# Kernel tuning notes

Hardware: AMD Instinct MI355X
Metric: run time of the kernel (lower is better)

## Reference

```python
import jax, jax.numpy as jnp
import numpy as np

EMBED = 1024
HEADS = 16
HEAD_DIM = EMBED // HEADS


def setup_inputs() -> dict:
    key = jax.random.key(0)
    k1, k2, k3, k4, k5 = jax.random.split(key, 5)
    B, S, E = 4, 2048, EMBED
    scale = 1.0 / np.sqrt(E)
    return {
        "tensor": jax.random.normal(k1, (B, S, E), dtype=jnp.float32),
        "in_proj_w": jax.random.normal(k2, (3 * E, E), dtype=jnp.float32) * scale,
        "in_proj_b": jax.random.normal(k3, (3 * E,), dtype=jnp.float32) * 0.02,
        "out_proj_w": jax.random.normal(k4, (E, E), dtype=jnp.float32) * scale,
        "out_proj_b": jax.random.normal(k5, (E,), dtype=jnp.float32) * 0.02,
        "causal_mask": 1,
    }


def reference(tensor, in_proj_w, in_proj_b, out_proj_w, out_proj_b, causal_mask):
    B, S, E = tensor.shape
    H, D = HEADS, HEAD_DIM
    # fused qkv projection (torch Linear: x @ W.T + b)
    qkv = tensor @ in_proj_w.T + in_proj_b  # [B, S, 3E]
    q, k, v = jnp.split(qkv, 3, axis=-1)
    # [B, S, E] -> [B, H, S, D]
    q = q.reshape(B, S, H, D).transpose(0, 2, 1, 3)
    k = k.reshape(B, S, H, D).transpose(0, 2, 1, 3)
    v = v.reshape(B, S, H, D).transpose(0, 2, 1, 3)
    scores = jnp.einsum("bhqd,bhkd->bhqk", q, k)  # [B, H, S, S]
    if causal_mask:
        mask = jnp.triu(jnp.ones((S, S), dtype=bool), k=1)
        scores = jnp.where(mask, -jnp.inf, scores)
    scores = scores / np.sqrt(D).astype(np.float32)
    attn = jax.nn.softmax(scores, axis=-1)
    out = jnp.einsum("bhqk,bhkd->bhqd", attn, v)  # [B, H, S, D]
    out = out.transpose(0, 2, 1, 3).reshape(B, S, E)
    return out @ out_proj_w.T + out_proj_b
```

## Files before the change

### kernel.cpp

```cpp
#include <hip/hip_runtime.h>
#include <hip/hip_bf16.h>

#define B_  4
#define S_  2048
#define E_  1024
#define H_  16
#define D_  64
#define M_  (B_*S_)
#define N3_ (3*E_)

typedef __bf16 bf16;
typedef bf16  bf16x4 __attribute__((ext_vector_type(4)));
typedef bf16  bf16x8 __attribute__((ext_vector_type(8)));
typedef float f32x4  __attribute__((ext_vector_type(4)));

#define SC2 0.18033688011112043f

__device__ __forceinline__ f32x4 mfma16(bf16x8 a, bf16x8 b, f32x4 c) {
    return __builtin_amdgcn_mfma_f32_16x16x32_bf16(a, b, c, 0, 0, 0);
}

typedef const __attribute__((address_space(1))) void* gas_t;
typedef __attribute__((address_space(3))) void* las_t;
__device__ __forceinline__ void gl_lds16(const void* g, void* l) {
    __builtin_amdgcn_global_load_lds((gas_t)g, (las_t)l, 16, 0, 0);
}

#define WAITCNT_VM4() __builtin_amdgcn_s_waitcnt(0x0F74)
#define WAITCNT_VM2() __builtin_amdgcn_s_waitcnt(0x0F72)
#define WAITCNT_VM0() __builtin_amdgcn_s_waitcnt(0x0F70)

__global__ __launch_bounds__(256) void cvt_all(const float* __restrict__ x,
                                               const float* __restrict__ w_in,
                                               const float* __restrict__ w_out,
                                               bf16* __restrict__ Xbf,
                                               bf16* __restrict__ Wqkv,
                                               bf16* __restrict__ Wo) {
    const int n1 = M_ * E_ / 4, n2 = N3_ * E_ / 4, n3 = E_ * E_ / 4;
    int i = blockIdx.x * blockDim.x + threadIdx.x;
    const float* src; bf16* dst; int j;
    if (i < n1)           { src = x;     dst = Xbf;  j = i; }
    else if (i < n1 + n2) { src = w_in;  dst = Wqkv; j = i - n1; }
    else if (i < n1 + n2 + n3) { src = w_out; dst = Wo; j = i - n1 - n2; }
    else return;
    float4 v = *(const float4*)(src + (size_t)j * 4);
    bf16x4 o;
    o[0] = (bf16)v.x; o[1] = (bf16)v.y; o[2] = (bf16)v.z; o[3] = (bf16)v.w;
    *(bf16x4*)(dst + (size_t)j * 4) = o;
}

__global__ __launch_bounds__(256) void gemm_qkv(const bf16* __restrict__ X,
                                                const bf16* __restrict__ W,
                                                const float* __restrict__ bias,
                                                bf16* __restrict__ QKV,
                                                bf16* __restrict__ Vt) {
    __shared__ __align__(16) bf16 As[128 * 64];
    __shared__ __align__(16) bf16 Bs[128 * 64];
    const int t = threadIdx.x;
    const int wav = t >> 6, lane = t & 63, quad = lane >> 4, l15 = lane & 15;
    const int m0 = blockIdx.y * 128, n0 = blockIdx.x * 128;
    const int wr = (wav >> 1) * 64, wc = (wav & 1) * 64;
    const int srow = t >> 3;
    const int swz  = ((t & 7) ^ (srow & 7)) * 8;
    const bool isV = (n0 >= 2 * E_);

    const bf16* Ablk = X + (size_t)m0 * E_;
    const bf16* Bblk = W + (size_t)n0 * E_;
    f32x4 acc[4][4] = {};

    for (int kk = 0; kk < E_; kk += 64) {
        __syncthreads();
        #pragma unroll
        for (int ps = 0; ps < 4; ++ps) {
            gl_lds16(Ablk + (size_t)(srow + ps * 32) * E_ + kk + swz, As + (size_t)(t + ps * 256) * 8);
            gl_lds16(Bblk + (size_t)(srow + ps * 32) * E_ + kk + swz, Bs + (size_t)(t + ps * 256) * 8);
        }
        __syncthreads();
        #pragma unroll
        for (int ks = 0; ks < 2; ++ks) {
            bf16x8 af[4], bw[4];
            #pragma unroll
            for (int i = 0; i < 4; ++i) {
                const int ra = wr + i * 16 + l15;
                const int rb = wc + i * 16 + l15;
                const int cx = ((ks * 4 + quad) ^ (l15 & 7)) * 8;
                af[i] = *(const bf16x8*)&As[ra * 64 + cx];
                bw[i] = *(const bf16x8*)&Bs[rb * 64 + cx];
            }
            if (!isV) {
                #pragma unroll
                for (int i = 0; i < 4; ++i)
                    #pragma unroll
                    for (int j = 0; j < 4; ++j)
                        acc[i][j] = mfma16(af[i], bw[j], acc[i][j]);
            } else {
                #pragma unroll
                for (int i = 0; i < 4; ++i)
                    #pragma unroll
                    for (int j = 0; j < 4; ++j)
                        acc[i][j] = mfma16(bw[i], af[j], acc[i][j]);
            }
        }
    }
    if (!isV) {
        #pragma unroll
        for (int i = 0; i < 4; ++i)
            #pragma unroll
            for (int j = 0; j < 4; ++j)
                #pragma unroll
                for (int r = 0; r < 4; ++r) {
                    int mg = m0 + wr + i * 16 + quad * 4 + r;
                    int ng = n0 + wc + j * 16 + l15;
                    float v = acc[i][j][r] + bias[ng];
                    int which = ng >> 10, rem = ng & 1023;
                    if (which == 0) v *= SC2;
                    int h = rem >> 6, d = rem & 63;
                    int b = mg >> 11, s = mg & 2047;
                    QKV[(size_t)which * (B_ * H_ * S_ * D_) +
                        (((size_t)(b * H_ + h) * S_ + s) * D_ + d)] = (bf16)v;
                }
    } else {
        #pragma unroll
        for (int i = 0; i < 4; ++i)
            #pragma unroll
            for (int j = 0; j < 4; ++j)
                #pragma unroll
                for (int r = 0; r < 4; ++r) {
                    int ng = n0 + wc + i * 16 + quad * 4 + r;
                    int mg = m0 + wr + j * 16 + l15;
                    float v = acc[i][j][r] + bias[ng];
                    int rem = ng & 1023;
                    int h = rem >> 6, d = rem & 63;
                    int b = mg >> 11, s = mg & 2047;
                    Vt[(((size_t)(b * H_ + h) * D_ + d) * S_) + s] = (bf16)v;
                }
    }
}

__global__ __launch_bounds__(512, 4) void attn8(const bf16* __restrict__ Q,
                                                const bf16* __restrict__ K,
                                                const bf16* __restrict__ Vt,
                                                bf16* __restrict__ O) {
    __shared__ __align__(16) bf16 Ks[2][64 * 64];
    __shared__ __align__(16) bf16 Vs[2][64 * 64];
    __shared__ __align__(16) bf16 Ps[8][16 * 64];

    const int t = threadIdx.x;
    const int wav = t >> 6, lane = t & 63, quad = lane >> 4, l15 = lane & 15;
    const int p  = blockIdx.x >> 6;
    const int bh = blockIdx.x & 63;

    const bf16* Qb = Q  + (size_t)bh * S_ * D_;
    const bf16* Kb = K  + (size_t)bh * S_ * D_;
    const bf16* Vb = Vt + (size_t)bh * (size_t)D_ * S_;

    const int srow = t >> 3;
    const int swz  = ((t & 7) ^ (srow & 7)) * 8;
    bf16* Pw = &Ps[wav][0];
    const int pswz = l15 & 7;

    const int b = bh >> 4, h = bh & 15;

    #pragma unroll 1
    for (int phase = 0; phase < 2; ++phase) {
        const int qb  = phase ? (15 - p) : p;
        const int q0w = qb * 128 + wav * 16;
        const int qg  = q0w + l15;
        const int niter = 2 * qb + 2;

        __builtin_amdgcn_s_barrier();
        gl_lds16(Kb + (size_t)srow * D_ + swz, &Ks[0][(size_t)t * 8]);
        gl_lds16(Vb + (size_t)srow * S_ + swz, &Vs[0][(size_t)t * 8]);

        bf16x8 qf0 = *(const bf16x8*)&Qb[(size_t)(q0w + l15) * D_ + quad * 8];
        bf16x8 qf1 = *(const bf16x8*)&Qb[(size_t)(q0w + l15) * D_ + 32 + quad * 8];

        f32x4 oacc[4] = {};
        f32x4 psum = {0.f, 0.f, 0.f, 0.f};

        #pragma unroll 1
        for (int it = 0; it < niter; ++it) {
            const int key0 = it * 64;
            const int cur = it & 1;
            const bf16* Kc = &Ks[cur][0];
            const bf16* Vc = &Vs[cur][0];

            __builtin_amdgcn_s_barrier();
            if (it + 1 < niter) {
                const int kn = key0 + 64;
                gl_lds16(Kb + (size_t)(kn + srow) * D_ + swz, &Ks[1 - cur][(size_t)t * 8]);
                gl_lds16(Vb + (size_t)srow * S_ + kn + swz,   &Vs[1 - cur][(size_t)t * 8]);
                WAITCNT_VM2();
            } else {
                WAITCNT_VM0();
            }
            __builtin_amdgcn_s_barrier();

            f32x4 sacc[4];
            #pragma unroll
            for (int mt = 0; mt < 4; ++mt) {
                const int krow = mt * 16 + l15;
                const int sw = krow & 7;
                bf16x8 kf0 = *(const bf16x8*)&Kc[krow * 64 + ((quad ^ sw) * 8)];
                bf16x8 kf1 = *(const bf16x8*)&Kc[krow * 64 + (((4 + quad) ^ sw) * 8)];
                f32x4 a = {};
                a = mfma16(kf0, qf0, a);
                a = mfma16(kf1, qf1, a);
                sacc[mt] = a;
            }

            #pragma unroll
            for (int mt = 0; mt < 4; ++mt) {
                if (key0 + mt * 16 + 15 > q0w) {
                    #pragma unroll
                    for (int r = 0; r < 4; ++r) {
                        int key = key0 + mt * 16 + quad * 4 + r;
                        sacc[mt][r] = (key > qg) ? -3e38f : sacc[mt][r];
                    }
                }
            }

            #pragma unroll
            for (int mt = 0; mt < 4; ++mt) {
                bf16x4 pk;
                #pragma unroll
                for (int r = 0; r < 4; ++r) {
                    float pv = __builtin_amdgcn_exp2f(sacc[mt][r]);
                    psum[r] += pv;
                    pk[r] = (bf16)pv;
                }
                const int pc = ((mt * 2 + (quad >> 1)) ^ pswz) * 8 + (quad & 1) * 4;
                *(bf16x4*)&Pw[l15 * 64 + pc] = pk;
            }

            bf16x8 pf0 = *(const bf16x8*)&Pw[l15 * 64 + ((quad ^ pswz) * 8)];
            bf16x8 pf1 = *(const bf16x8*)&Pw[l15 * 64 + (((4 + quad) ^ pswz) * 8)];
            #pragma unroll
            for (int nt = 0; nt < 4; ++nt) {
                const int vrow = nt * 16 + l15;
                const int sw = vrow & 7;
                bf16x8 vf0 = *(const bf16x8*)&Vc[vrow * 64 + ((quad ^ sw) * 8)];
                bf16x8 vf1 = *(const bf16x8*)&Vc[vrow * 64 + (((4 + quad) ^ sw) * 8)];
                oacc[nt] = mfma16(pf0, vf0, oacc[nt]);
                oacc[nt] = mfma16(pf1, vf1, oacc[nt]);
            }
        }

        float rsum = psum[0] + psum[1] + psum[2] + psum[3];
        rsum += __shfl_xor(rsum, 16);
        rsum += __shfl_xor(rsum, 32);
        const float linv = 1.0f / rsum;

        #pragma unroll
        for (int rr = 0; rr < 4; ++rr) {
            float li = __shfl(linv, quad * 4 + rr);
            const int q = q0w + quad * 4 + rr;
            #pragma unroll
            for (int nt = 0; nt < 4; ++nt)
                O[((size_t)b * S_ + q) * E_ + h * D_ + nt * 16 + l15] =
                    (bf16)(oacc[nt][rr] * li);
        }
    }
}

__global__ __launch_bounds__(256) void gemm_out(const bf16* __restrict__ A,
                                                const bf16* __restrict__ W,
                                                const float* __restrict__ bias,
                                                float* __restrict__ out) {
    __shared__ __align__(16) bf16 As[128 * 64];
    __shared__ __align__(16) bf16 Bs[128 * 64];
    const int t = threadIdx.x;
    const int wav = t >> 6, lane = t & 63, quad = lane >> 4, l15 = lane & 15;
    const int m0 = blockIdx.y * 128, n0 = blockIdx.x * 128;
    const int wr = (wav >> 1) * 64, wc = (wav & 1) * 64;
    const int srow = t >> 3;
    const int swz  = ((t & 7) ^ (srow & 7)) * 8;

    const bf16* Ablk = A + (size_t)m0 * E_;
    const bf16* Bblk = W + (size_t)n0 * E_;
    f32x4 acc[4][4] = {};

    for (int kk = 0; kk < E_; kk += 64) {
        __syncthreads();
        #pragma unroll
        for (int ps = 0; ps < 4; ++ps) {
            gl_lds16(Ablk + (size_t)(srow + ps * 32) * E_ + kk + swz, As + (size_t)(t + ps * 256) * 8);
            gl_lds16(Bblk + (size_t)(srow + ps * 32) * E_ + kk + swz, Bs + (size_t)(t + ps * 256) * 8);
        }
        __syncthreads();
        #pragma unroll
        for (int ks = 0; ks < 2; ++ks) {
            bf16x8 af[4], bw[4];
            #pragma unroll
            for (int i = 0; i < 4; ++i) {
                const int ra = wr + i * 16 + l15;
                const int rb = wc + i * 16 + l15;
                const int cx = ((ks * 4 + quad) ^ (l15 & 7)) * 8;
                af[i] = *(const bf16x8*)&As[ra * 64 + cx];
                bw[i] = *(const bf16x8*)&Bs[rb * 64 + cx];
            }
            #pragma unroll
            for (int i = 0; i < 4; ++i)
                #pragma unroll
                for (int j = 0; j < 4; ++j)
                    acc[i][j] = mfma16(af[i], bw[j], acc[i][j]);
        }
    }
    #pragma unroll
    for (int i = 0; i < 4; ++i)
        #pragma unroll
        for (int j = 0; j < 4; ++j)
            #pragma unroll
            for (int r = 0; r < 4; ++r) {
                int mg = m0 + wr + i * 16 + quad * 4 + r;
                int ng = n0 + wc + j * 16 + l15;
                out[(size_t)mg * E_ + ng] = acc[i][j][r] + bias[ng];
            }
}

extern "C" void kernel_launch(void* const* d_in, const int* in_sizes, int n_in,
                              void* d_out, int out_size, void* d_ws, size_t ws_size,
                              hipStream_t stream) {
    const float* x     = (const float*)d_in[0];
    const float* w_in  = (const float*)d_in[1];
    const float* b_in  = (const float*)d_in[2];
    const float* w_out = (const float*)d_in[3];
    const float* b_out = (const float*)d_in[4];
    float* out = (float*)d_out;

    char* ws = (char*)d_ws;
    bf16* Xbf  = (bf16*)ws; ws += (size_t)M_ * E_ * 2;
    bf16* Wqkv = (bf16*)ws; ws += (size_t)N3_ * E_ * 2;
    bf16* Wo   = (bf16*)ws; ws += (size_t)E_ * E_ * 2;
    bf16* QKV  = (bf16*)ws; ws += (size_t)2 * B_ * H_ * S_ * D_ * 2;
    bf16* Vt   = (bf16*)ws; ws += (size_t)B_ * H_ * S_ * D_ * 2;
    bf16* Obf  = Xbf;

    const int nCvt = (M_ * E_ + N3_ * E_ + E_ * E_) / 4;
    cvt_all<<<(nCvt + 255) / 256, 256, 0, stream>>>(x, w_in, w_out, Xbf, Wqkv, Wo);

    gemm_qkv<<<dim3(N3_ / 128, M_ / 128), 256, 0, stream>>>(Xbf, Wqkv, b_in, QKV, Vt);

    bf16* Qp = QKV;
    bf16* Kp = QKV + (size_t)B_ * H_ * S_ * D_;

    attn8<<<dim3(8 * B_ * H_), 512, 0, stream>>>(Qp, Kp, Vt, Obf);

    gemm_out<<<dim3(E_ / 128, M_ / 128), 256, 0, stream>>>(Obf, Wo, b_out, out);
}
```

Baseline: 233.1 us.

## Triple-buffer GEMM mainloops with 256x128 tiles and 512-thread blocks

Both projection GEMMs move to 256x128 block tiles run by 8 waves, with a three-stage LDS ring loaded through global_load_lds. Prefetch of tile k+2 is split across two MFMA phases, and s_waitcnt vmcnt plus s_barrier and s_setprio are used so loads overlap with compute. The aim is to hide global-memory latency and reuse each B tile across twice as many rows. In exchange it needs 144 KB of LDS per block, which limits occupancy, and the gemm_out grid shrinks to 256 blocks.

Measured after the change: 229.4 us. Within noise of the previous version (-1.6%).

```diff
diff --git a/kernel.cpp b/kernel.cpp
--- a/kernel.cpp
+++ b/kernel.cpp
@@ -26,7 +26,6 @@
     __builtin_amdgcn_global_load_lds((gas_t)g, (las_t)l, 16, 0, 0);
 }
 
-#define WAITCNT_VM4() __builtin_amdgcn_s_waitcnt(0x0F74)
 #define WAITCNT_VM2() __builtin_amdgcn_s_waitcnt(0x0F72)
 #define WAITCNT_VM0() __builtin_amdgcn_s_waitcnt(0x0F70)
 
@@ -49,17 +48,82 @@
     *(bf16x4*)(dst + (size_t)j * 4) = o;
 }
 
-__global__ __launch_bounds__(256) void gemm_qkv(const bf16* __restrict__ X,
-                                                const bf16* __restrict__ W,
-                                                const float* __restrict__ bias,
-                                                bf16* __restrict__ QKV,
-                                                bf16* __restrict__ Vt) {
-    __shared__ __align__(16) bf16 As[128 * 64];
-    __shared__ __align__(16) bf16 Bs[128 * 64];
+
+#define STG_A(dst, kk, ps) gl_lds16(Ablk + (size_t)(srow + (ps)*64)*E_ + (kk) + swz, (dst) + (size_t)(t + (ps)*512)*8)
+#define STG_B(dst, kk, ps) gl_lds16(Bblk + (size_t)(srow + (ps)*64)*E_ + (kk) + swz, (dst) + (size_t)(t + (ps)*512)*8)
+#define LDF(base, row, ks) (*(const bf16x8*)&(base)[(row)*64 + ((((ks)*4 + quad) ^ ((row)&7))*8)])
+
+#define MFMA_PHASE(p, ISV)                                                     \
+    if (!(ISV)) {                                                              \
+        _Pragma("unroll") for (int i2 = 0; i2 < 2; ++i2)                       \
+            _Pragma("unroll") for (int j = 0; j < 4; ++j) {                    \
+                acc[2*(p)+i2][j] = mfma16(af[i2][0], bw[j][0], acc[2*(p)+i2][j]); \
+                acc[2*(p)+i2][j] = mfma16(af[i2][1], bw[j][1], acc[2*(p)+i2][j]); \
+            }                                                                  \
+    } else {                                                                   \
+        _Pragma("unroll") for (int j = 0; j < 4; ++j)                          \
+            _Pragma("unroll") for (int i2 = 0; i2 < 2; ++i2) {                 \
+                acc[j][2*(p)+i2] = mfma16(bw[j][0], af[i2][0], acc[j][2*(p)+i2]); \
+                acc[j][2*(p)+i2] = mfma16(bw[j][1], af[i2][1], acc[j][2*(p)+i2]); \
+            }                                                                  \
+    }
+
+#define GEMM_MAINLOOP(ISV)                                                     \
+    {                                                                          \
+        bf16 *Ac = &As[0][0], *An = &As[1][0], *Af = &As[2][0];                \
+        bf16 *Bc = &Bs[0][0], *Bn = &Bs[1][0], *Bf = &Bs[2][0];                \
+                                   \
+        STG_A(Ac, 0, 0);  STG_A(Ac, 0, 1);  STG_A(Ac, 0, 2);  STG_A(Ac, 0, 3); \
+        STG_B(Bc, 0, 0);  STG_B(Bc, 0, 1);                                     \
+        STG_A(An, 64, 0); STG_A(An, 64, 1); STG_A(An, 64, 2); STG_A(An, 64, 3);\
+        STG_B(Bn, 64, 0); STG_B(Bn, 64, 1);                                    \
+        for (int kt = 0; kt < 16; ++kt) {                                      \
+            \
+            if (kt < 15) asm volatile("s_waitcnt vmcnt(6)\n\ts_barrier" ::: "memory"); \
+            else         asm volatile("s_waitcnt vmcnt(0)\n\ts_barrier" ::: "memory"); \
+            const int kk2 = (kt + 2) * 64;                                     \
+            const bool st = (kt < 14);                                         \
+            bf16x8 af[2][2], bw[4][2];                                         \
+                    \
+            _Pragma("unroll") for (int i2 = 0; i2 < 2; ++i2) {                 \
+                int ra = wro + i2 * 16 + l15;                                  \
+                af[i2][0] = LDF(Ac, ra, 0); af[i2][1] = LDF(Ac, ra, 1);        \
+            }                                                                  \
+            _Pragma("unroll") for (int j = 0; j < 4; ++j) {                    \
+                int rb = wco + j * 16 + l15;                                   \
+                bw[j][0] = LDF(Bc, rb, 0); bw[j][1] = LDF(Bc, rb, 1);          \
+            }                                                                  \
+            if (st) { STG_A(Af, kk2, 0); STG_A(Af, kk2, 1); STG_B(Bf, kk2, 0); } \
+            __builtin_amdgcn_s_setprio(1);                                     \
+            MFMA_PHASE(0, ISV)                                                 \
+            __builtin_amdgcn_s_setprio(0);                                     \
+            asm volatile("s_barrier" ::: "memory");                            \
+                            \
+            _Pragma("unroll") for (int i2 = 0; i2 < 2; ++i2) {                 \
+                int ra = wro + (2 + i2) * 16 + l15;                            \
+                af[i2][0] = LDF(Ac, ra, 0); af[i2][1] = LDF(Ac, ra, 1);        \
+            }                                                                  \
+            if (st) { STG_A(Af, kk2, 2); STG_A(Af, kk2, 3); STG_B(Bf, kk2, 1); } \
+            __builtin_amdgcn_s_setprio(1);                                     \
+            MFMA_PHASE(1, ISV)                                                 \
+            __builtin_amdgcn_s_setprio(0);                                     \
+            bf16* tp;                                                          \
+            tp = Ac; Ac = An; An = Af; Af = tp;                                \
+            tp = Bc; Bc = Bn; Bn = Bf; Bf = tp;                                \
+        }                                                                      \
+    }
+
+__global__ __launch_bounds__(512, 2) void gemm_qkv(const bf16* __restrict__ X,
+                                                   const bf16* __restrict__ W,
+                                                   const float* __restrict__ bias,
+                                                   bf16* __restrict__ QKV,
+                                                   bf16* __restrict__ Vt) {
+    __shared__ __align__(16) bf16 As[3][256 * 64];
+    __shared__ __align__(16) bf16 Bs[3][128 * 64];
     const int t = threadIdx.x;
     const int wav = t >> 6, lane = t & 63, quad = lane >> 4, l15 = lane & 15;
-    const int m0 = blockIdx.y * 128, n0 = blockIdx.x * 128;
-    const int wr = (wav >> 1) * 64, wc = (wav & 1) * 64;
+    const int m0 = blockIdx.y * 256, n0 = blockIdx.x * 128;
+    const int wro = (wav >> 1) * 64, wco = (wav & 1) * 64;
     const int srow = t >> 3;
     const int swz  = ((t & 7) ^ (srow & 7)) * 8;
     const bool isV = (n0 >= 2 * E_);
@@ -68,40 +132,8 @@
     const bf16* Bblk = W + (size_t)n0 * E_;
     f32x4 acc[4][4] = {};
 
-    for (int kk = 0; kk < E_; kk += 64) {
-        __syncthreads();
-        #pragma unroll
-        for (int ps = 0; ps < 4; ++ps) {
-            gl_lds16(Ablk + (size_t)(srow + ps * 32) * E_ + kk + swz, As + (size_t)(t + ps * 256) * 8);
-            gl_lds16(Bblk + (size_t)(srow + ps * 32) * E_ + kk + swz, Bs + (size_t)(t + ps * 256) * 8);
-        }
-        __syncthreads();
-        #pragma unroll
-        for (int ks = 0; ks < 2; ++ks) {
-            bf16x8 af[4], bw[4];
-            #pragma unroll
-            for (int i = 0; i < 4; ++i) {
-                const int ra = wr + i * 16 + l15;
-                const int rb = wc + i * 16 + l15;
-                const int cx = ((ks * 4 + quad) ^ (l15 & 7)) * 8;
-                af[i] = *(const bf16x8*)&As[ra * 64 + cx];
-                bw[i] = *(const bf16x8*)&Bs[rb * 64 + cx];
-            }
-            if (!isV) {
-                #pragma unroll
-                for (int i = 0; i < 4; ++i)
-                    #pragma unroll
-                    for (int j = 0; j < 4; ++j)
-                        acc[i][j] = mfma16(af[i], bw[j], acc[i][j]);
-            } else {
-                #pragma unroll
-                for (int i = 0; i < 4; ++i)
-                    #pragma unroll
-                    for (int j = 0; j < 4; ++j)
-                        acc[i][j] = mfma16(bw[i], af[j], acc[i][j]);
-            }
-        }
-    }
+    GEMM_MAINLOOP(isV)
+
     if (!isV) {
         #pragma unroll
         for (int i = 0; i < 4; ++i)
@@ -109,8 +141,8 @@
             for (int j = 0; j < 4; ++j)
                 #pragma unroll
                 for (int r = 0; r < 4; ++r) {
-                    int mg = m0 + wr + i * 16 + quad * 4 + r;
-                    int ng = n0 + wc + j * 16 + l15;
+                    int mg = m0 + wro + i * 16 + quad * 4 + r;
+                    int ng = n0 + wco + j * 16 + l15;
                     float v = acc[i][j][r] + bias[ng];
                     int which = ng >> 10, rem = ng & 1023;
                     if (which == 0) v *= SC2;
@@ -126,8 +158,8 @@
             for (int j = 0; j < 4; ++j)
                 #pragma unroll
                 for (int r = 0; r < 4; ++r) {
-                    int ng = n0 + wc + i * 16 + quad * 4 + r;
-                    int mg = m0 + wr + j * 16 + l15;
+                    int ng = n0 + wco + i * 16 + quad * 4 + r;
+                    int mg = m0 + wro + j * 16 + l15;
                     float v = acc[i][j][r] + bias[ng];
                     int rem = ng & 1023;
                     int h = rem >> 6, d = rem & 63;
@@ -263,16 +295,16 @@
     }
 }
 
-__global__ __launch_bounds__(256) void gemm_out(const bf16* __restrict__ A,
-                                                const bf16* __restrict__ W,
-                                                const float* __restrict__ bias,
-                                                float* __restrict__ out) {
-    __shared__ __align__(16) bf16 As[128 * 64];
-    __shared__ __align__(16) bf16 Bs[128 * 64];
+__global__ __launch_bounds__(512, 2) void gemm_out(const bf16* __restrict__ A,
+                                                   const bf16* __restrict__ W,
+                                                   const float* __restrict__ bias,
+                                                   float* __restrict__ out) {
+    __shared__ __align__(16) bf16 As[3][256 * 64];
+    __shared__ __align__(16) bf16 Bs[3][128 * 64];
     const int t = threadIdx.x;
     const int wav = t >> 6, lane = t & 63, quad = lane >> 4, l15 = lane & 15;
-    const int m0 = blockIdx.y * 128, n0 = blockIdx.x * 128;
-    const int wr = (wav >> 1) * 64, wc = (wav & 1) * 64;
+    const int m0 = blockIdx.y * 256, n0 = blockIdx.x * 128;
+    const int wro = (wav >> 1) * 64, wco = (wav & 1) * 64;
     const int srow = t >> 3;
     const int swz  = ((t & 7) ^ (srow & 7)) * 8;
 
@@ -280,40 +312,16 @@
     const bf16* Bblk = W + (size_t)n0 * E_;
     f32x4 acc[4][4] = {};
 
-    for (int kk = 0; kk < E_; kk += 64) {
-        __syncthreads();
-        #pragma unroll
-        for (int ps = 0; ps < 4; ++ps) {
-            gl_lds16(Ablk + (size_t)(srow + ps * 32) * E_ + kk + swz, As + (size_t)(t + ps * 256) * 8);
-            gl_lds16(Bblk + (size_t)(srow + ps * 32) * E_ + kk + swz, Bs + (size_t)(t + ps * 256) * 8);
-        }
-        __syncthreads();
-        #pragma unroll
-        for (int ks = 0; ks < 2; ++ks) {
-            bf16x8 af[4], bw[4];
-            #pragma unroll
-            for (int i = 0; i < 4; ++i) {
-                const int ra = wr + i * 16 + l15;
-                const int rb = wc + i * 16 + l15;
-                const int cx = ((ks * 4 + quad) ^ (l15 & 7)) * 8;
-                af[i] = *(const bf16x8*)&As[ra * 64 + cx];
-                bw[i] = *(const bf16x8*)&Bs[rb * 64 + cx];
-            }
-            #pragma unroll
-            for (int i = 0; i < 4; ++i)
-                #pragma unroll
-                for (int j = 0; j < 4; ++j)
-                    acc[i][j] = mfma16(af[i], bw[j], acc[i][j]);
-        }
-    }
+    GEMM_MAINLOOP(false)
+
     #pragma unroll
     for (int i = 0; i < 4; ++i)
         #pragma unroll
         for (int j = 0; j < 4; ++j)
             #pragma unroll
             for (int r = 0; r < 4; ++r) {
-                int mg = m0 + wr + i * 16 + quad * 4 + r;
-                int ng = n0 + wc + j * 16 + l15;
+                int mg = m0 + wro + i * 16 + quad * 4 + r;
+                int ng = n0 + wco + j * 16 + l15;
                 out[(size_t)mg * E_ + ng] = acc[i][j][r] + bias[ng];
             }
 }
@@ -339,12 +347,12 @@
     const int nCvt = (M_ * E_ + N3_ * E_ + E_ * E_) / 4;
     cvt_all<<<(nCvt + 255) / 256, 256, 0, stream>>>(x, w_in, w_out, Xbf, Wqkv, Wo);
 
-    gemm_qkv<<<dim3(N3_ / 128, M_ / 128), 256, 0, stream>>>(Xbf, Wqkv, b_in, QKV, Vt);
+    gemm_qkv<<<dim3(N3_ / 128, M_ / 256), 512, 0, stream>>>(Xbf, Wqkv, b_in, QKV, Vt);
 
     bf16* Qp = QKV;
     bf16* Kp = QKV + (size_t)B_ * H_ * S_ * D_;
 
     attn8<<<dim3(8 * B_ * H_), 512, 0, stream>>>(Qp, Kp, Vt, Obf);
 
-    gemm_out<<<dim3(E_ / 128, M_ / 128), 256, 0, stream>>>(Obf, Wo, b_out, out);
-}
+    gemm_out<<<dim3(E_ / 128, M_ / 256), 512, 0, stream>>>(Obf, Wo, b_out, out);
+}
```

## Process two 16-row query tiles per wave in attention to reuse K/V fragments

Applied to the files above, without the earlier changes.

Each attention wave now handles 32 query rows (two 16-row MFMA tiles) instead of 16. Each block covers 256 queries and the grid is halved. Every K and V fragment read from LDS feeds twice as many MFMAs, which is meant to cut LDS traffic and per-key-tile overhead such as barriers and global-to-LDS loads. In exchange the kernel uses more registers and twice the P scratch in LDS, so the occupancy bound drops to 2, and the halved grid leaves about one 8-wave block per CU, which lowers latency hiding and load balance.

Measured after the change: 243.1 us. +4.3%, slower.

```diff
diff --git a/kernel.cpp b/kernel.cpp
--- a/kernel.cpp
+++ b/kernel.cpp
@@ -26,7 +26,6 @@
     __builtin_amdgcn_global_load_lds((gas_t)g, (las_t)l, 16, 0, 0);
 }
 
-#define WAITCNT_VM4() __builtin_amdgcn_s_waitcnt(0x0F74)
 #define WAITCNT_VM2() __builtin_amdgcn_s_waitcnt(0x0F72)
 #define WAITCNT_VM0() __builtin_amdgcn_s_waitcnt(0x0F70)
 
@@ -137,13 +136,13 @@
     }
 }
 
-__global__ __launch_bounds__(512, 4) void attn8(const bf16* __restrict__ Q,
+__global__ __launch_bounds__(512, 2) void attn8(const bf16* __restrict__ Q,
                                                 const bf16* __restrict__ K,
                                                 const bf16* __restrict__ Vt,
                                                 bf16* __restrict__ O) {
     __shared__ __align__(16) bf16 Ks[2][64 * 64];
     __shared__ __align__(16) bf16 Vs[2][64 * 64];
-    __shared__ __align__(16) bf16 Ps[8][16 * 64];
+    __shared__ __align__(16) bf16 Ps[8][32 * 64];
 
     const int t = threadIdx.x;
     const int wav = t >> 6, lane = t & 63, quad = lane >> 4, l15 = lane & 15;
@@ -163,20 +162,23 @@
 
     #pragma unroll 1
     for (int phase = 0; phase < 2; ++phase) {
-        const int qb  = phase ? (15 - p) : p;
-        const int q0w = qb * 128 + wav * 16;
-        const int qg  = q0w + l15;
-        const int niter = 2 * qb + 2;
+        const int qb  = phase ? (7 - p) : p;
+        const int q0w = qb * 256 + wav * 32;
+        const int niter = 4 * qb + 4;
 
         __builtin_amdgcn_s_barrier();
         gl_lds16(Kb + (size_t)srow * D_ + swz, &Ks[0][(size_t)t * 8]);
         gl_lds16(Vb + (size_t)srow * S_ + swz, &Vs[0][(size_t)t * 8]);
 
-        bf16x8 qf0 = *(const bf16x8*)&Qb[(size_t)(q0w + l15) * D_ + quad * 8];
-        bf16x8 qf1 = *(const bf16x8*)&Qb[(size_t)(q0w + l15) * D_ + 32 + quad * 8];
-
-        f32x4 oacc[4] = {};
-        f32x4 psum = {0.f, 0.f, 0.f, 0.f};
+        bf16x8 qf[2][2];
+        #pragma unroll
+        for (int qi = 0; qi < 2; ++qi) {
+            qf[qi][0] = *(const bf16x8*)&Qb[(size_t)(q0w + qi * 16 + l15) * D_ + quad * 8];
+            qf[qi][1] = *(const bf16x8*)&Qb[(size_t)(q0w + qi * 16 + l15) * D_ + 32 + quad * 8];
+        }
+
+        f32x4 oacc[2][4] = {};
+        f32x4 psum[2] = {};
 
         #pragma unroll 1
         for (int it = 0; it < niter; ++it) {
@@ -196,69 +198,89 @@
             }
             __builtin_amdgcn_s_barrier();
 
-            f32x4 sacc[4];
+            f32x4 sacc[2][4];
             #pragma unroll
             for (int mt = 0; mt < 4; ++mt) {
                 const int krow = mt * 16 + l15;
                 const int sw = krow & 7;
                 bf16x8 kf0 = *(const bf16x8*)&Kc[krow * 64 + ((quad ^ sw) * 8)];
                 bf16x8 kf1 = *(const bf16x8*)&Kc[krow * 64 + (((4 + quad) ^ sw) * 8)];
-                f32x4 a = {};
-                a = mfma16(kf0, qf0, a);
-                a = mfma16(kf1, qf1, a);
-                sacc[mt] = a;
-            }
-
-            #pragma unroll
-            for (int mt = 0; mt < 4; ++mt) {
-                if (key0 + mt * 16 + 15 > q0w) {
+                #pragma unroll
+                for (int qi = 0; qi < 2; ++qi) {
+                    f32x4 a = {};
+                    a = mfma16(kf0, qf[qi][0], a);
+                    a = mfma16(kf1, qf[qi][1], a);
+                    sacc[qi][mt] = a;
+                }
+            }
+
+            #pragma unroll
+            for (int qi = 0; qi < 2; ++qi) {
+                const int qg = q0w + qi * 16 + l15;
+                #pragma unroll
+                for (int mt = 0; mt < 4; ++mt) {
+                    if (key0 + mt * 16 + 15 > q0w + qi * 16) {
+                        #pragma unroll
+                        for (int r = 0; r < 4; ++r) {
+                            int key = key0 + mt * 16 + quad * 4 + r;
+                            sacc[qi][mt][r] = (key > qg) ? -3e38f : sacc[qi][mt][r];
+                        }
+                    }
+                }
+            }
+
+            #pragma unroll
+            for (int qi = 0; qi < 2; ++qi) {
+                #pragma unroll
+                for (int mt = 0; mt < 4; ++mt) {
+                    bf16x4 pk;
                     #pragma unroll
                     for (int r = 0; r < 4; ++r) {
-                        int key = key0 + mt * 16 + quad * 4 + r;
-                        sacc[mt][r] = (key > qg) ? -3e38f : sacc[mt][r];
+                        float pv = __builtin_amdgcn_exp2f(sacc[qi][mt][r]);
+                        psum[qi][r] += pv;
+                        pk[r] = (bf16)pv;
                     }
-                }
-            }
-
-            #pragma unroll
-            for (int mt = 0; mt < 4; ++mt) {
-                bf16x4 pk;
-                #pragma unroll
-                for (int r = 0; r < 4; ++r) {
-                    float pv = __builtin_amdgcn_exp2f(sacc[mt][r]);
-                    psum[r] += pv;
-                    pk[r] = (bf16)pv;
-                }
-                const int pc = ((mt * 2 + (quad >> 1)) ^ pswz) * 8 + (quad & 1) * 4;
-                *(bf16x4*)&Pw[l15 * 64 + pc] = pk;
-            }
-
-            bf16x8 pf0 = *(const bf16x8*)&Pw[l15 * 64 + ((quad ^ pswz) * 8)];
-            bf16x8 pf1 = *(const bf16x8*)&Pw[l15 * 64 + (((4 + quad) ^ pswz) * 8)];
+                    const int pc = ((mt * 2 + (quad >> 1)) ^ pswz) * 8 + (quad & 1) * 4;
+                    *(bf16x4*)&Pw[(qi * 16 + l15) * 64 + pc] = pk;
+                }
+            }
+
+            bf16x8 pf[2][2];
+            #pragma unroll
+            for (int qi = 0; qi < 2; ++qi) {
+                pf[qi][0] = *(const bf16x8*)&Pw[(qi * 16 + l15) * 64 + ((quad ^ pswz) * 8)];
+                pf[qi][1] = *(const bf16x8*)&Pw[(qi * 16 + l15) * 64 + (((4 + quad) ^ pswz) * 8)];
+            }
             #pragma unroll
             for (int nt = 0; nt < 4; ++nt) {
                 const int vrow = nt * 16 + l15;
                 const int sw = vrow & 7;
                 bf16x8 vf0 = *(const bf16x8*)&Vc[vrow * 64 + ((quad ^ sw) * 8)];
                 bf16x8 vf1 = *(const bf16x8*)&Vc[vrow * 64 + (((4 + quad) ^ sw) * 8)];
-                oacc[nt] = mfma16(pf0, vf0, oacc[nt]);
-                oacc[nt] = mfma16(pf1, vf1, oacc[nt]);
-            }
-        }
-
-        float rsum = psum[0] + psum[1] + psum[2] + psum[3];
-        rsum += __shfl_xor(rsum, 16);
-        rsum += __shfl_xor(rsum, 32);
-        const float linv = 1.0f / rsum;
-
-        #pragma unroll
-        for (int rr = 0; rr < 4; ++rr) {
-            float li = __shfl(linv, quad * 4 + rr);
-            const int q = q0w + quad * 4 + rr;
-            #pragma unroll
-            for (int nt = 0; nt < 4; ++nt)
-                O[((size_t)b * S_ + q) * E_ + h * D_ + nt * 16 + l15] =
-                    (bf16)(oacc[nt][rr] * li);
+                #pragma unroll
+                for (int qi = 0; qi < 2; ++qi) {
+                    oacc[qi][nt] = mfma16(pf[qi][0], vf0, oacc[qi][nt]);
+                    oacc[qi][nt] = mfma16(pf[qi][1], vf1, oacc[qi][nt]);
+                }
+            }
+        }
+
+        #pragma unroll
+        for (int qi = 0; qi < 2; ++qi) {
+            float rsum = psum[qi][0] + psum[qi][1] + psum[qi][2] + psum[qi][3];
+            rsum += __shfl_xor(rsum, 16);
+            rsum += __shfl_xor(rsum, 32);
+            const float linv = 1.0f / rsum;
+
+            #pragma unroll
+            for (int rr = 0; rr < 4; ++rr) {
+                float li = __shfl(linv, quad * 4 + rr);
+                const int q = q0w + qi * 16 + quad * 4 + rr;
+                #pragma unroll
+                for (int nt = 0; nt < 4; ++nt)
+                    O[((size_t)b * S_ + q) * E_ + h * D_ + nt * 16 + l15] =
+                        (bf16)(oacc[qi][nt][rr] * li);
+            }
         }
     }
 }
@@ -344,7 +366,7 @@
     bf16* Qp = QKV;
     bf16* Kp = QKV + (size_t)B_ * H_ * S_ * D_;
 
-    attn8<<<dim3(8 * B_ * H_), 512, 0, stream>>>(Qp, Kp, Vt, Obf);
+    attn8<<<dim3(4 * B_ * H_), 512, 0, stream>>>(Qp, Kp, Vt, Obf);
 
     gemm_out<<<dim3(E_ / 128, M_ / 128), 256, 0, stream>>>(Obf, Wo, b_out, out);
 }
```

## Double key tile in attention and triple-buffer pipelined out-projection GEMM

Applied to the files above, without the earlier changes.

The attention kernel now stages 128-key K/V tiles per iteration, processed as two 64-key halves. This halves the barrier and load-issue count per query block, and fully masked halves are skipped. The output projection GEMM moves to 256x128 tiles with 512 threads and a three-stage LDS ring buffer. Global-to-LDS loads for tile k+2 are interleaved with MFMA work, and setprio raises priority around the MFMA blocks. This costs more LDS per block, which may lower occupancy, and the manual vmcnt waits must match the number of outstanding loads exactly.

Result: no change. 232.2 us (-0.4%).

```diff
diff --git a/kernel.cpp b/kernel.cpp
--- a/kernel.cpp
+++ b/kernel.cpp
@@ -27,7 +27,6 @@
 }
 
 #define WAITCNT_VM4() __builtin_amdgcn_s_waitcnt(0x0F74)
-#define WAITCNT_VM2() __builtin_amdgcn_s_waitcnt(0x0F72)
 #define WAITCNT_VM0() __builtin_amdgcn_s_waitcnt(0x0F70)
 
 __global__ __launch_bounds__(256) void cvt_all(const float* __restrict__ x,
@@ -141,8 +140,8 @@
                                                 const bf16* __restrict__ K,
                                                 const bf16* __restrict__ Vt,
                                                 bf16* __restrict__ O) {
-    __shared__ __align__(16) bf16 Ks[2][64 * 64];
-    __shared__ __align__(16) bf16 Vs[2][64 * 64];
+    __shared__ __align__(16) bf16 Ks[2][128 * 64];
+    __shared__ __align__(16) bf16 Vs[2][64 * 128];
     __shared__ __align__(16) bf16 Ps[8][16 * 64];
 
     const int t = threadIdx.x;
@@ -154,8 +153,12 @@
     const bf16* Kb = K  + (size_t)bh * S_ * D_;
     const bf16* Vb = Vt + (size_t)bh * (size_t)D_ * S_;
 
-    const int srow = t >> 3;
-    const int swz  = ((t & 7) ^ (srow & 7)) * 8;
+    const int kr0 = t >> 3;
+    const int kswz = ((t & 7) ^ (kr0 & 7)) * 8;
+    const int vr0 = t >> 4;
+    const int vc  = t & 15;
+    const int vkey = ((vc >> 3) * 64) + (((vc & 7) ^ (vr0 & 7)) * 8);
+
     bf16* Pw = &Ps[wav][0];
     const int pswz = l15 & 7;
 
@@ -166,11 +169,13 @@
         const int qb  = phase ? (15 - p) : p;
         const int q0w = qb * 128 + wav * 16;
         const int qg  = q0w + l15;
-        const int niter = 2 * qb + 2;
+        const int niter = qb + 1;
 
         __builtin_amdgcn_s_barrier();
-        gl_lds16(Kb + (size_t)srow * D_ + swz, &Ks[0][(size_t)t * 8]);
-        gl_lds16(Vb + (size_t)srow * S_ + swz, &Vs[0][(size_t)t * 8]);
+        gl_lds16(Kb + (size_t)kr0 * D_ + kswz,        &Ks[0][(size_t)t * 8]);
+        gl_lds16(Kb + (size_t)(kr0 + 64) * D_ + kswz, &Ks[0][(size_t)(t + 512) * 8]);
+        gl_lds16(Vb + (size_t)vr0 * S_ + vkey,        &Vs[0][(size_t)t * 8]);
+        gl_lds16(Vb + (size_t)(vr0 + 32) * S_ + vkey, &Vs[0][(size_t)(t + 512) * 8]);
 
         bf16x8 qf0 = *(const bf16x8*)&Qb[(size_t)(q0w + l15) * D_ + quad * 8];
         bf16x8 qf1 = *(const bf16x8*)&Qb[(size_t)(q0w + l15) * D_ + 32 + quad * 8];
@@ -180,69 +185,77 @@
 
         #pragma unroll 1
         for (int it = 0; it < niter; ++it) {
-            const int key0 = it * 64;
+            const int key0 = it * 128;
             const int cur = it & 1;
             const bf16* Kc = &Ks[cur][0];
             const bf16* Vc = &Vs[cur][0];
 
             __builtin_amdgcn_s_barrier();
             if (it + 1 < niter) {
-                const int kn = key0 + 64;
-                gl_lds16(Kb + (size_t)(kn + srow) * D_ + swz, &Ks[1 - cur][(size_t)t * 8]);
-                gl_lds16(Vb + (size_t)srow * S_ + kn + swz,   &Vs[1 - cur][(size_t)t * 8]);
-                WAITCNT_VM2();
+                const int kn = key0 + 128;
+                bf16* Kd = &Ks[1 - cur][0];
+                bf16* Vd = &Vs[1 - cur][0];
+                gl_lds16(Kb + (size_t)(kn + kr0) * D_ + kswz,        &Kd[(size_t)t * 8]);
+                gl_lds16(Kb + (size_t)(kn + kr0 + 64) * D_ + kswz,   &Kd[(size_t)(t + 512) * 8]);
+                gl_lds16(Vb + (size_t)vr0 * S_ + kn + vkey,          &Vd[(size_t)t * 8]);
+                gl_lds16(Vb + (size_t)(vr0 + 32) * S_ + kn + vkey,   &Vd[(size_t)(t + 512) * 8]);
+                WAITCNT_VM4();
             } else {
                 WAITCNT_VM0();
             }
             __builtin_amdgcn_s_barrier();
 
-            f32x4 sacc[4];
-            #pragma unroll
-            for (int mt = 0; mt < 4; ++mt) {
-                const int krow = mt * 16 + l15;
-                const int sw = krow & 7;
-                bf16x8 kf0 = *(const bf16x8*)&Kc[krow * 64 + ((quad ^ sw) * 8)];
-                bf16x8 kf1 = *(const bf16x8*)&Kc[krow * 64 + (((4 + quad) ^ sw) * 8)];
-                f32x4 a = {};
-                a = mfma16(kf0, qf0, a);
-                a = mfma16(kf1, qf1, a);
-                sacc[mt] = a;
-            }
-
-            #pragma unroll
-            for (int mt = 0; mt < 4; ++mt) {
-                if (key0 + mt * 16 + 15 > q0w) {
+            #pragma unroll
+            for (int hh = 0; hh < 2; ++hh) {
+                const int key0h = key0 + hh * 64;
+                if (key0h > q0w + 15) continue;
+
+                f32x4 sacc[4];
+                #pragma unroll
+                for (int mt = 0; mt < 4; ++mt) {
+                    const int krow = hh * 64 + mt * 16 + l15;
+                    bf16x8 kf0 = *(const bf16x8*)&Kc[krow * 64 + ((quad ^ pswz) * 8)];
+                    bf16x8 kf1 = *(const bf16x8*)&Kc[krow * 64 + (((4 + quad) ^ pswz) * 8)];
+                    f32x4 a = {};
+                    a = mfma16(kf0, qf0, a);
+                    a = mfma16(kf1, qf1, a);
+                    sacc[mt] = a;
+                }
+
+                #pragma unroll
+                for (int mt = 0; mt < 4; ++mt) {
+                    if (key0h + mt * 16 + 15 > q0w) {
+                        #pragma unroll
+                        for (int r = 0; r < 4; ++r) {
+                            int key = key0h + mt * 16 + quad * 4 + r;
+                            sacc[mt][r] = (key > qg) ? -3e38f : sacc[mt][r];
+                        }
+                    }
+                }
+
+                #pragma unroll
+                for (int mt = 0; mt < 4; ++mt) {
+                    bf16x4 pk;
                     #pragma unroll
                     for (int r = 0; r < 4; ++r) {
-                        int key = key0 + mt * 16 + quad * 4 + r;
-                        sacc[mt][r] = (key > qg) ? -3e38f : sacc[mt][r];
+                        float pv = __builtin_amdgcn_exp2f(sacc[mt][r]);
+                        psum[r] += pv;
+                        pk[r] = (bf16)pv;
                     }
-                }
-            }
-
-            #pragma unroll
-            for (int mt = 0; mt < 4; ++mt) {
-                bf16x4 pk;
-                #pragma unroll
-                for (int r = 0; r < 4; ++r) {
-                    float pv = __builtin_amdgcn_exp2f(sacc[mt][r]);
-                    psum[r] += pv;
-                    pk[r] = (bf16)pv;
-                }
-                const int pc = ((mt * 2 + (quad >> 1)) ^ pswz) * 8 + (quad & 1) * 4;
-                *(bf16x4*)&Pw[l15 * 64 + pc] = pk;
-            }
-
-            bf16x8 pf0 = *(const bf16x8*)&Pw[l15 * 64 + ((quad ^ pswz) * 8)];
-            bf16x8 pf1 = *(const bf16x8*)&Pw[l15 * 64 + (((4 + quad) ^ pswz) * 8)];
-            #pragma unroll
-            for (int nt = 0; nt < 4; ++nt) {
-                const int vrow = nt * 16 + l15;
-                const int sw = vrow & 7;
-                bf16x8 vf0 = *(const bf16x8*)&Vc[vrow * 64 + ((quad ^ sw) * 8)];
-                bf16x8 vf1 = *(const bf16x8*)&Vc[vrow * 64 + (((4 + quad) ^ sw) * 8)];
-                oacc[nt] = mfma16(pf0, vf0, oacc[nt]);
-                oacc[nt] = mfma16(pf1, vf1, oacc[nt]);
+                    const int pc = ((mt * 2 + (quad >> 1)) ^ pswz) * 8 + (quad & 1) * 4;
+                    *(bf16x4*)&Pw[l15 * 64 + pc] = pk;
+                }
+
+                bf16x8 pf0 = *(const bf16x8*)&Pw[l15 * 64 + ((quad ^ pswz) * 8)];
+                bf16x8 pf1 = *(const bf16x8*)&Pw[l15 * 64 + (((4 + quad) ^ pswz) * 8)];
+                #pragma unroll
+                for (int nt = 0; nt < 4; ++nt) {
+                    const int vrow = nt * 16 + l15;
+                    bf16x8 vf0 = *(const bf16x8*)&Vc[vrow * 128 + ((hh * 8 + (quad ^ pswz)) * 8)];
+                    bf16x8 vf1 = *(const bf16x8*)&Vc[vrow * 128 + ((hh * 8 + ((4 + quad) ^ pswz)) * 8)];
+                    oacc[nt] = mfma16(pf0, vf0, oacc[nt]);
+                    oacc[nt] = mfma16(pf1, vf1, oacc[nt]);
+                }
             }
         }
 
@@ -263,16 +276,20 @@
     }
 }
 
-__global__ __launch_bounds__(256) void gemm_out(const bf16* __restrict__ A,
-                                                const bf16* __restrict__ W,
-                                                const float* __restrict__ bias,
-                                                float* __restrict__ out) {
-    __shared__ __align__(16) bf16 As[128 * 64];
-    __shared__ __align__(16) bf16 Bs[128 * 64];
+#define STG_A(dst, kk, ps) gl_lds16(Ablk + (size_t)(srow + (ps)*64)*E_ + (kk) + swz, (dst) + (size_t)(t + (ps)*512)*8)
+#define STG_B(dst, kk, ps) gl_lds16(Bblk + (size_t)(srow + (ps)*64)*E_ + (kk) + swz, (dst) + (size_t)(t + (ps)*512)*8)
+#define LDF(base, row, ks) (*(const bf16x8*)&(base)[(row)*64 + ((((ks)*4 + quad) ^ ((row)&7))*8)])
+
+__global__ __launch_bounds__(512, 2) void gemm_out(const bf16* __restrict__ A,
+                                                   const bf16* __restrict__ W,
+                                                   const float* __restrict__ bias,
+                                                   float* __restrict__ out) {
+    __shared__ __align__(16) bf16 As[3][256 * 64];
+    __shared__ __align__(16) bf16 Bs[3][128 * 64];
     const int t = threadIdx.x;
     const int wav = t >> 6, lane = t & 63, quad = lane >> 4, l15 = lane & 15;
-    const int m0 = blockIdx.y * 128, n0 = blockIdx.x * 128;
-    const int wr = (wav >> 1) * 64, wc = (wav & 1) * 64;
+    const int m0 = blockIdx.y * 256, n0 = blockIdx.x * 128;
+    const int wro = (wav >> 1) * 64, wco = (wav & 1) * 64;
     const int srow = t >> 3;
     const int swz  = ((t & 7) ^ (srow & 7)) * 8;
 
@@ -280,40 +297,69 @@
     const bf16* Bblk = W + (size_t)n0 * E_;
     f32x4 acc[4][4] = {};
 
-    for (int kk = 0; kk < E_; kk += 64) {
-        __syncthreads();
-        #pragma unroll
-        for (int ps = 0; ps < 4; ++ps) {
-            gl_lds16(Ablk + (size_t)(srow + ps * 32) * E_ + kk + swz, As + (size_t)(t + ps * 256) * 8);
-            gl_lds16(Bblk + (size_t)(srow + ps * 32) * E_ + kk + swz, Bs + (size_t)(t + ps * 256) * 8);
-        }
-        __syncthreads();
-        #pragma unroll
-        for (int ks = 0; ks < 2; ++ks) {
-            bf16x8 af[4], bw[4];
-            #pragma unroll
-            for (int i = 0; i < 4; ++i) {
-                const int ra = wr + i * 16 + l15;
-                const int rb = wc + i * 16 + l15;
-                const int cx = ((ks * 4 + quad) ^ (l15 & 7)) * 8;
-                af[i] = *(const bf16x8*)&As[ra * 64 + cx];
-                bw[i] = *(const bf16x8*)&Bs[rb * 64 + cx];
-            }
-            #pragma unroll
-            for (int i = 0; i < 4; ++i)
-                #pragma unroll
-                for (int j = 0; j < 4; ++j)
-                    acc[i][j] = mfma16(af[i], bw[j], acc[i][j]);
+    {
+        bf16 *Ac = &As[0][0], *An = &As[1][0], *Af = &As[2][0];
+        bf16 *Bc = &Bs[0][0], *Bn = &Bs[1][0], *Bf = &Bs[2][0];
+        STG_A(Ac, 0, 0);  STG_A(Ac, 0, 1);  STG_A(Ac, 0, 2);  STG_A(Ac, 0, 3);
+        STG_B(Bc, 0, 0);  STG_B(Bc, 0, 1);
+        STG_A(An, 64, 0); STG_A(An, 64, 1); STG_A(An, 64, 2); STG_A(An, 64, 3);
+        STG_B(Bn, 64, 0); STG_B(Bn, 64, 1);
+        for (int kt = 0; kt < 16; ++kt) {
+            if (kt < 15) asm volatile("s_waitcnt vmcnt(6)\n\ts_barrier" ::: "memory");
+            else         asm volatile("s_waitcnt vmcnt(0)\n\ts_barrier" ::: "memory");
+            const int kk2 = (kt + 2) * 64;
+            const bool st = (kt < 14);
+            bf16x8 af[2][2], bw[4][2];
+            #pragma unroll
+            for (int i2 = 0; i2 < 2; ++i2) {
+                int ra = wro + i2 * 16 + l15;
+                af[i2][0] = LDF(Ac, ra, 0); af[i2][1] = LDF(Ac, ra, 1);
+            }
+            #pragma unroll
+            for (int j = 0; j < 4; ++j) {
+                int rb = wco + j * 16 + l15;
+                bw[j][0] = LDF(Bc, rb, 0); bw[j][1] = LDF(Bc, rb, 1);
+            }
+            if (st) { STG_A(Af, kk2, 0); STG_A(Af, kk2, 1); STG_B(Bf, kk2, 0); }
+            __builtin_amdgcn_s_setprio(1);
+            #pragma unroll
+            for (int i2 = 0; i2 < 2; ++i2)
+                #pragma unroll
+                for (int j = 0; j < 4; ++j) {
+                    acc[i2][j] = mfma16(af[i2][0], bw[j][0], acc[i2][j]);
+                    acc[i2][j] = mfma16(af[i2][1], bw[j][1], acc[i2][j]);
+                }
+            __builtin_amdgcn_s_setprio(0);
+            asm volatile("s_barrier" ::: "memory");
+            #pragma unroll
+            for (int i2 = 0; i2 < 2; ++i2) {
+                int ra = wro + (2 + i2) * 16 + l15;
+                af[i2][0] = LDF(Ac, ra, 0); af[i2][1] = LDF(Ac, ra, 1);
+            }
+            if (st) { STG_A(Af, kk2, 2); STG_A(Af, kk2, 3); STG_B(Bf, kk2, 1); }
+            __builtin_amdgcn_s_setprio(1);
+            #pragma unroll
+            for (int i2 = 0; i2 < 2; ++i2)
+                #pragma unroll
+                for (int j = 0; j < 4; ++j) {
+                    acc[2 + i2][j] = mfma16(af[i2][0], bw[j][0], acc[2 + i2][j]);
+                    acc[2 + i2][j] = mfma16(af[i2][1], bw[j][1], acc[2 + i2][j]);
+                }
+            __builtin_amdgcn_s_setprio(0);
+            bf16* tp;
+            tp = Ac; Ac = An; An = Af; Af = tp;
+            tp = Bc; Bc = Bn; Bn = Bf; Bf = tp;
         }
     }
+
     #pragma unroll
     for (int i = 0; i < 4; ++i)
         #pragma unroll
         for (int j = 0; j < 4; ++j)
             #pragma unroll
             for (int r = 0; r < 4; ++r) {
-                int mg = m0 + wr + i * 16 + quad * 4 + r;
-                int ng = n0 + wc + j * 16 + l15;
+                int mg = m0 + wro + i * 16 + quad * 4 + r;
+                int ng = n0 + wco + j * 16 + l15;
                 out[(size_t)mg * E_ + ng] = acc[i][j][r] + bias[ng];
             }
 }
@@ -346,5 +392,5 @@
 
     attn8<<<dim3(8 * B_ * H_), 512, 0, stream>>>(Qp, Kp, Vt, Obf);
 
-    gemm_out<<<dim3(E_ / 128, M_ / 128), 256, 0, stream>>>(Obf, Wo, b_out, out);
-}
+    gemm_out<<<dim3(E_ / 128, M_ / 256), 512, 0, stream>>>(Obf, Wo, b_out, out);
+}
```
